# Kernel tuning notes

Measured on AMD Instinct MI355X. Metric: run time of the kernel, lower is better.

## Reference

```python
import jax, jax.numpy as jnp
import numpy as np
from functools import partial

B, C, FD, H, W = 8, 256, 128, 64, 64
POSC = 34  # 32 learned pos channels + 2 raw meshgrid channels


def create_meshgrid(h, w):
    # kornia-style normalized grid in [-1, 1], returned as [1, 2, h, w] (x, y)
    xs = jnp.linspace(-1.0, 1.0, w, dtype=jnp.float32)
    ys = jnp.linspace(-1.0, 1.0, h, dtype=jnp.float32)
    gy, gx = jnp.meshgrid(ys, xs, indexing='ij')
    return jnp.stack([gx, gy], axis=0)[None]  # [1,2,h,w]


def conv1x1(x, w, b):
    return jnp.einsum('bchw,oc->bohw', x, w) + b[None, :, None, None]


def pos_gen(feat, pg_w1, pg_b1, pg_w2, pg_b2):
    # PosGen type=2 with detach: two 1x1 'mul' layers (conv + ReLU, no norm)
    b, c, h, w = feat.shape
    feat = jax.lax.stop_gradient(feat)
    pos = jnp.broadcast_to(create_meshgrid(h, w), (b, 2, h, w))
    inp = jnp.concatenate([pos + 1.0, feat], axis=1)           # [b, feat_dim+2, h, w]
    h1 = jax.nn.relu(conv1x1(inp, pg_w1, pg_b1))               # [b, feat_dim, h, w]
    h2 = jax.nn.relu(conv1x1(h1, pg_w2, pg_b2))                # [b, 32, h, w]
    return jnp.concatenate([h2, pos], axis=1)                  # [b, 34, h, w]


def fuser(x, feat, w1, b1, w2, b2):
    # fuser_1D: concat along channels, 1x1 -> hidden (ReLU) -> 1x1 -> 256
    z = jnp.concatenate([x, feat], axis=1)
    z = jax.nn.relu(conv1x1(z, w1, b1))
    return conv1x1(z, w2, b2)


def conv_y(y, dw_w, dw_b, pw_w, pw_b):
    # BasicDWLayer: depthwise 3x3 + pointwise 1x1, no norm, no activation
    z = jax.lax.conv_general_dilated(
        y, dw_w, window_strides=(1, 1), padding='SAME',
        feature_group_count=y.shape[1],
        dimension_numbers=('NCHW', 'OIHW', 'NCHW')) + dw_b[None, :, None, None]
    return conv1x1(z, pw_w, pw_b)


def matching_forward(x, y, feat1, feat2,
                     pg_w1, pg_b1, pg_w2, pg_b2,
                     fus_w1, fus_b1, fus_w2, fus_b2,
                     dw_w, dw_b, pw_w, pw_b,
                     dustbin_vec, dustbin_pos):
    b, c, hx, wx = x.shape
    hy, wy = y.shape[2], y.shape[3]

    posf = pos_gen(feat2, pg_w1, pg_b1, pg_w2, pg_b2)          # [b, 34, hy, wy]
    c_pose = posf.shape[1]
    pos = posf.reshape(b, 1, c_pose, hy * wy).swapaxes(-1, -2)  # [b,1,Nk,34]

    xf = fuser(x, feat1, fus_w1, fus_b1, fus_w2, fus_b2)
    yf = fuser(y, feat2, fus_w1, fus_b1, fus_w2, fus_b2)
    yf = conv_y(yf, dw_w, dw_b, pw_w, pw_b)
    d = yf.shape[1]

    q = xf.reshape(b, 1, d, hx * wx).swapaxes(-1, -2)           # [b,1,Nq,256]
    k = yf.reshape(b, 1, d, hy * wy).swapaxes(-1, -2)           # [b,1,Nk,256]

    # dustbin token augmentation
    k = jnp.concatenate([k, jnp.broadcast_to(dustbin_vec, (b, 1, 1, d))], axis=-2)
    pos = jnp.concatenate([pos, jnp.broadcast_to(dustbin_pos, (b, 1, 1, c_pose))], axis=-2)

    # single-head cross-attention: values are the positional channels
    scores = jnp.einsum('bhqc,bhkc->bhqk', q, k) / jnp.sqrt(jnp.float32(d))
    attn = jax.nn.softmax(scores, axis=-1)
    out = jnp.einsum('bhqk,bhkd->bhqd', attn, pos)              # [b,1,Nq,34]
    return out.swapaxes(-1, -2).reshape(b, c_pose, hx, wx)


def setup_inputs() -> dict:
    key = jax.random.key(0)
    ks = jax.random.split(key, 20)
    s = 0.05
    return {
        'x': jax.random.normal(ks[0], (B, C, H, W), jnp.float32),
        'y': jax.random.normal(ks[1], (B, C, H, W), jnp.float32),
        'feat1': jax.random.normal(ks[2], (B, FD, H, W), jnp.float32),
        'feat2': jax.random.normal(ks[3], (B, FD, H, W), jnp.float32),
        # PosGen type-2 mapping: (feat_dim+2)->feat_dim, feat_dim->(hidden-2=32)
        'pg_w1': jax.random.normal(ks[4], (FD, FD + 2), jnp.float32) * s,
        'pg_b1': jnp.zeros((FD,), jnp.float32),
        'pg_w2': jax.random.normal(ks[5], (32, FD), jnp.float32) * s,
        'pg_b2': jnp.zeros((32,), jnp.float32),
        # fuser_1D: (256+128)->256 hidden, hidden->256
        'fus_w1': jax.random.normal(ks[6], (256, C + FD), jnp.float32) * s,
        'fus_b1': jnp.zeros((256,), jnp.float32),
        'fus_w2': jax.random.normal(ks[7], (C, 256), jnp.float32) * s,
        'fus_b2': jnp.zeros((C,), jnp.float32),
        # conv_y: depthwise 3x3 + pointwise 1x1
        'dw_w': jax.random.normal(ks[8], (C, 1, 3, 3), jnp.float32) * s,
        'dw_b': jnp.zeros((C,), jnp.float32),
        'pw_w': jax.random.normal(ks[9], (C, C), jnp.float32) * s,
        'pw_b': jnp.zeros((C,), jnp.float32),
        'dustbin_vec': jax.random.uniform(ks[10], (1, 1, 1, C), jnp.float32) / 10.0,
        'dustbin_pos': jnp.zeros((1, 1, 1, POSC), jnp.float32) - 10.0,
    }


def reference(x, y, feat1, feat2,
              pg_w1, pg_b1, pg_w2, pg_b2,
              fus_w1, fus_b1, fus_w2, fus_b2,
              dw_w, dw_b, pw_w, pw_b,
              dustbin_vec, dustbin_pos):
    return matching_forward(x, y, feat1, feat2,
                            pg_w1, pg_b1, pg_w2, pg_b2,
                            fus_w1, fus_b1, fus_w2, fus_b2,
                            dw_w, dw_b, pw_w, pw_b,
                            dustbin_vec, dustbin_pos)
```

## Files before the change

### kernel.cpp

```cpp
#include <hip/hip_runtime.h>
#include <hip/hip_bf16.h>

typedef __hip_bfloat16 bf16;
typedef unsigned short ushort_t;
typedef __bf16 bf16x8 __attribute__((ext_vector_type(8)));
typedef float  f32x4  __attribute__((ext_vector_type(4)));

#define HW    4096
#define NB    8
#define KSTR  4160
#define NTOK  32768
#define PROWS 64
#define QSCALE 0.0901684400557f

__device__ __forceinline__ float lde(const void* p, size_t i, int f32f) {
    return f32f ? ((const float*)p)[i] : (float)((const bf16*)p)[i];
}
__device__ __forceinline__ ushort_t f2bu(float f){ union { __bf16 b; ushort_t u; } cv; cv.b = (__bf16)f; return cv.u; }

__device__ __forceinline__ void async_cp16(const void* g, void* l) {
    __builtin_amdgcn_global_load_lds(
        (const __attribute__((address_space(1))) unsigned int*)g,
        (__attribute__((address_space(3))) unsigned int*)l, 16, 0, 0);
}

__global__ void detect_kernel(const ushort_t* xb, int* flag)
{
    __shared__ int cnt;
    const int t = threadIdx.x;
    if (t == 0) cnt = 0;
    __syncthreads();
    ushort_t h = xb[2*t];
    int e = (h >> 7) & 0xFF;
    if (e >= 133) atomicAdd(&cnt, 1);
    __syncthreads();
    if (t == 0) *flag = (cnt > 8) ? 1 : 0;
}

struct WsPtrs {
    bf16 *fw1t, *fw2t, *pwt, *pgw1t, *pgw2t, *dwt, *pos;
    float *posw, *fb1, *fb2, *pwb, *pgb1, *pgb2, *dwb;
};

__global__ __launch_bounds__(256) void prep_kernel(
    const void* fus_w1, const void* fus_w2, const void* pw_w,
    const void* pg_w1, const void* pg_w2, const void* dw_w,
    const void* fus_b1, const void* fus_b2, const void* pw_b,
    const void* pg_b1, const void* pg_b2, const void* dw_b,
    const void* dpos, WsPtrs W, const int* flag)
{
    const int f = *flag;
    const long n_w1 = 98304, n_w2 = 65536, n_pw = 65536, n_g1 = 16384, n_g2 = 4096;
    const long n_posw = 256, n_dwt = 2304;
    const long n_b = 256, n_gb1 = 128, n_gb2 = 32;
    const long n_mesh = 65536;
    const long n_pad  = 8L*14*KSTR;
    const long n_dust = 272;
    const long n_zt   = 8L*34*63;
    const long total = n_w1+n_w2+n_pw+n_g1+n_g2+n_posw+n_dwt
                     + 3*n_b + n_gb1 + n_gb2 + n_b + n_mesh + n_pad + n_dust + n_zt;

    for (long i = blockIdx.x*256L + threadIdx.x; i < total; i += gridDim.x*256L) {
        long j = i;
        if (j < n_w1) { W.fw1t[j] = __float2bfloat16(lde(fus_w1, j, f)); continue; } j -= n_w1;
        if (j < n_w2) { W.fw2t[j] = __float2bfloat16(lde(fus_w2, j, f)); continue; } j -= n_w2;
        if (j < n_pw) { W.pwt[j]  = __float2bfloat16(lde(pw_w,  j, f)); continue; } j -= n_pw;
        if (j < n_g1) { W.pgw1t[j] = __float2bfloat16(lde(pg_w1, (j>>7)*130 + 2 + (j&127), f)); continue; } j -= n_g1;
        if (j < n_g2) { W.pgw2t[j] = __float2bfloat16(lde(pg_w2, j, f)); continue; } j -= n_g2;
        if (j < n_posw) { W.posw[j] = lde(pg_w1, (j>>1)*130 + (j&1), f); continue; } j -= n_posw;
        if (j < n_dwt) { W.dwt[j] = __float2bfloat16(lde(dw_w, (j&255)*9 + (j>>8), f)); continue; } j -= n_dwt;
        if (j < n_b)   { W.fb1[j] = lde(fus_b1, j, f); continue; } j -= n_b;
        if (j < n_b)   { W.fb2[j] = lde(fus_b2, j, f); continue; } j -= n_b;
        if (j < n_b)   { W.pwb[j] = lde(pw_b, j, f); continue; } j -= n_b;
        if (j < n_gb1) { W.pgb1[j] = lde(pg_b1, j, f); continue; } j -= n_gb1;
        if (j < n_gb2) { W.pgb2[j] = lde(pg_b2, j, f); continue; } j -= n_gb2;
        if (j < n_b)   { W.dwb[j] = lde(dw_b, j, f); continue; } j -= n_b;
        if (j < n_mesh) {
            long b = j >> 13; int rr = (int)((j>>12)&1); int tok = (int)(j & 4095);
            float v = rr ? (-1.f + 2.f*(float)((tok>>6)&63)/63.f)
                         : (-1.f + 2.f*(float)(tok&63)/63.f);
            W.pos[((size_t)b*PROWS + 32 + rr)*KSTR + tok] = __float2bfloat16(v);
            continue;
        } j -= n_mesh;
        if (j < n_pad) {
            long b = j / (14L*KSTR); long rem = j % (14L*KSTR);
            int row = 34 + (int)(rem / KSTR); int tok = (int)(rem % KSTR);
            W.pos[((size_t)b*PROWS + row)*KSTR + tok] = __float2bfloat16(row == 34 ? 1.f : 0.f);
            continue;
        } j -= n_pad;
        if (j < n_dust) {
            long b = j / 34; int ch = (int)(j % 34);
            W.pos[((size_t)b*PROWS + ch)*KSTR + 4096] = __float2bfloat16(lde(dpos, ch, f));
            continue;
        } j -= n_dust;
        { long b = j / (34*63); long rem = j % (34*63);
          int ch = (int)(rem / 63); int cc = (int)(rem % 63);
          W.pos[((size_t)b*PROWS + ch)*KSTR + 4097 + cc] = __float2bfloat16(0.f); }
    }
}

__global__ __launch_bounds__(256) void transpose_kernel(
    const void* main_src, const void* feat_src, bf16* __restrict__ dst, const int* flag)
{
    __shared__ float Tt[64*65];
    const int t = threadIdx.x;
    const int p0 = blockIdx.x * 64;
    const int cht = blockIdx.y;
    const int b = blockIdx.z;
    const int f = *flag;

    const void* src; int ch0, srcC, dc0;
    if (cht < 4) { src = main_src; ch0 = cht*64; srcC = 256; dc0 = ch0; }
    else         { src = feat_src; ch0 = (cht-4)*64; srcC = 128; dc0 = 256 + (cht-4)*64; }

    const int p = t & 63, cq = t >> 6;
    #pragma unroll
    for (int e = 0; e < 16; ++e) {
        int c = e*4 + cq;
        Tt[p*65 + c] = lde(src, ((size_t)b*srcC + ch0 + c)*HW + p0 + p, f);
    }
    __syncthreads();
    const int pr = t >> 2, cs = (t & 3) * 16;
    union { uint4 u4[2]; ushort_t us[16]; } pk;
    #pragma unroll
    for (int u = 0; u < 16; ++u) pk.us[u] = f2bu(Tt[pr*65 + cs + u]);
    ushort_t* op = (ushort_t*)dst + ((size_t)b*HW + p0 + pr)*384 + dc0 + cs;
    *(uint4*)op = pk.u4[0];
    *((uint4*)op + 1) = pk.u4[1];
}

template<int MT, bool RELU, bool POSEPI, int OMODE>
__global__ __launch_bounds__(256) void gemm_mfma(
    const bf16* __restrict__ A, int sa,
    const bf16* __restrict__ Bw, int ldb,
    const float* __restrict__ bias, const float* __restrict__ posw,
    bf16* __restrict__ out, int sm, int K, float oscale)
{
    const int t = threadIdx.x;
    const int w = t >> 6, lane = t & 63;
    const int n = lane & 15, quad = lane >> 4;
    const int p0 = blockIdx.x * 128;
    const int m0 = blockIdx.y * (MT*16);
    const int rowbase = p0 + w*32;

    f32x4 acc[2][MT];
    #pragma unroll
    for (int pt = 0; pt < 2; ++pt)
        #pragma unroll
        for (int mt = 0; mt < MT; ++mt) acc[pt][mt] = (f32x4){0.f,0.f,0.f,0.f};

    for (int k0 = 0; k0 < K; k0 += 32) {
        bf16x8 ap[2];
        #pragma unroll
        for (int pt = 0; pt < 2; ++pt)
            ap[pt] = *(const bf16x8*)&A[(size_t)(rowbase + pt*16 + n)*sa + k0 + quad*8];
        #pragma unroll
        for (int mt = 0; mt < MT; ++mt) {
            bf16x8 bw = *(const bf16x8*)&Bw[(size_t)(m0 + mt*16 + n)*ldb + k0 + quad*8];
            acc[0][mt] = __builtin_amdgcn_mfma_f32_16x16x32_bf16(ap[0], bw, acc[0][mt], 0, 0, 0);
            acc[1][mt] = __builtin_amdgcn_mfma_f32_16x16x32_bf16(ap[1], bw, acc[1][mt], 0, 0, 0);
        }
    }

    #pragma unroll
    for (int mt = 0; mt < MT; ++mt) {
        const int m = m0 + mt*16 + n;
        const float bi = bias[m];
        float w0 = 0.f, w1 = 0.f;
        if (POSEPI) { w0 = posw[m*2]; w1 = posw[m*2 + 1]; }
        #pragma unroll
        for (int pt = 0; pt < 2; ++pt) {
            const int tokb = rowbase + pt*16 + quad*4;
            if (OMODE == 1) {
                union { uint2 u2; ushort_t us[4]; } pk;
                #pragma unroll
                for (int r = 0; r < 4; ++r) {
                    float v = acc[pt][mt][r] + bi;
                    if (RELU) v = fmaxf(v, 0.f);
                    pk.us[r] = f2bu(v * oscale);
                }
                size_t oi = ((size_t)(tokb >> 12)*PROWS + m)*KSTR + (tokb & 4095);
                *(uint2*)((ushort_t*)out + oi) = pk.u2;
            } else {
                #pragma unroll
                for (int r = 0; r < 4; ++r) {
                    int tok = tokb + r;
                    float v = acc[pt][mt][r] + bi;
                    if (POSEPI) {
                        float gx1 = 2.f * (float)(tok & 63) / 63.f;
                        float gy1 = 2.f * (float)((tok >> 6) & 63) / 63.f;
                        v += w0*gx1 + w1*gy1;
                    }
                    if (RELU) v = fmaxf(v, 0.f);
                    v *= oscale;
                    size_t row = (OMODE == 2) ? (size_t)tok + 64*(size_t)(tok >> 12) : (size_t)tok;
                    out[row*sm + m] = __float2bfloat16(v);
                }
            }
        }
    }
}

__global__ __launch_bounds__(256) void dw_kernel(
    const bf16* __restrict__ in, const bf16* __restrict__ dwt,
    const float* __restrict__ dwb, bf16* __restrict__ out)
{
    const int t = threadIdx.x;
    const int tok = blockIdx.x*8 + (t >> 5);
    const int c8 = (t & 31) * 8;
    const int b = tok >> 12, p = tok & 4095;
    const int i = p >> 6, j = p & 63;

    float acc[8];
    #pragma unroll
    for (int u = 0; u < 8; ++u) acc[u] = dwb[c8 + u];

    #pragma unroll
    for (int di = 0; di < 3; ++di) {
        int ii = i + di - 1;
        if (ii < 0 || ii >= 64) continue;
        #pragma unroll
        for (int dj = 0; dj < 3; ++dj) {
            int jj = j + dj - 1;
            if (jj < 0 || jj >= 64) continue;
            int tok2 = (b << 12) + ii*64 + jj;
            bf16x8 xv = *(const bf16x8*)&in[(size_t)tok2*256 + c8];
            bf16x8 wv = *(const bf16x8*)&dwt[(di*3 + dj)*256 + c8];
            #pragma unroll
            for (int u = 0; u < 8; ++u) acc[u] += (float)xv[u] * (float)wv[u];
        }
    }
    union { uint4 u4; ushort_t us[8]; } pk;
    #pragma unroll
    for (int u = 0; u < 8; ++u) pk.us[u] = f2bu(acc[u]);
    *(uint4*)((ushort_t*)out + (size_t)tok*256 + c8) = pk.u4;
}

__global__ __launch_bounds__(256) void fill_late_kernel(
    const void* dvec, bf16* __restrict__ k_t, const int* flag)
{
    const int b = blockIdx.x, t = threadIdx.x;
    k_t[((size_t)b*KSTR + 4096)*256 + t] = __float2bfloat16(lde(dvec, t, *flag));
}

__global__ __launch_bounds__(256, 2) void attn_kernel(
    const bf16* __restrict__ q_t, const bf16* __restrict__ k_t,
    const bf16* __restrict__ pos, void* outv, const int* flag)
{
    __shared__ __align__(16) __bf16 Ks[2048*8];
    __shared__ __align__(16) __bf16 posb[512*8];
    __shared__ __align__(16) __bf16 Pb[64*72];

    const int t = threadIdx.x;
    const int w = t >> 6, lane = t & 63;
    const int n = lane & 15, quad = lane >> 4;
    const int qt = blockIdx.x, b = blockIdx.y;

    bf16x8 aq[8];
    {
        size_t qrow = (size_t)b*HW + qt*64 + w*16 + n;
        #pragma unroll
        for (int c = 0; c < 8; ++c)
            aq[c] = *(const bf16x8*)&q_t[qrow*256 + c*32 + quad*8];
    }

    f32x4 pacc[3];
    #pragma unroll
    for (int ct = 0; ct < 3; ++ct) pacc[ct] = (f32x4){0.f,0.f,0.f,0.f};

    const ushort_t* ksrc0 = (const ushort_t*)k_t + (size_t)b*KSTR*256;
    const ushort_t* psrc0 = (const ushort_t*)pos + (size_t)b*PROWS*KSTR;
    const int xw = n & 7;

    for (int kt = 0; kt < 65; ++kt) {
        const int kbase = kt*64;

        __syncthreads();
        #pragma unroll
        for (int e = 0; e < 8; ++e) {
            int slot = w*512 + e*64 + lane;
            int tok = slot >> 5;
            int ch = ((slot & 31) ^ (tok & 7)) * 8;
            async_cp16(&ksrc0[(size_t)(kbase + tok)*256 + ch], &Ks[(size_t)slot*8]);
        }
        #pragma unroll
        for (int e = 0; e < 2; ++e) {
            int slot = w*128 + e*64 + lane;
            int row = slot >> 3;
            int ch = ((slot & 7) ^ (row & 7)) * 8;
            async_cp16(&psrc0[(size_t)row*KSTR + kbase + ch], &posb[(size_t)slot*8]);
        }
        __syncthreads();

        f32x4 sacc[4];
        #pragma unroll
        for (int nt = 0; nt < 4; ++nt) sacc[nt] = (f32x4){0.f,0.f,0.f,0.f};
        #pragma unroll
        for (int c = 0; c < 8; ++c) {
            #pragma unroll
            for (int nt = 0; nt < 4; ++nt) {
                bf16x8 bk = *(const bf16x8*)&Ks[(size_t)((nt*16 + n)*32 + ((c*4 + quad) ^ xw))*8];
                sacc[nt] = __builtin_amdgcn_mfma_f32_16x16x32_bf16(aq[c], bk, sacc[nt], 0, 0, 0);
            }
        }

        #pragma unroll
        for (int nt = 0; nt < 4; ++nt) {
            const bool ok = (kbase + nt*16 + n) <= 4096;
            #pragma unroll
            for (int r = 0; r < 4; ++r) {
                float pv = ok ? __builtin_amdgcn_exp2f(sacc[nt][r]) : 0.f;
                Pb[(w*16 + quad*4 + r)*72 + nt*16 + n] = (__bf16)pv;
            }
        }

        #pragma unroll
        for (int c = 0; c < 2; ++c) {
            bf16x8 aP = *(const bf16x8*)&Pb[(w*16 + n)*72 + c*32 + quad*8];
            #pragma unroll
            for (int ct = 0; ct < 3; ++ct) {
                bf16x8 bp = *(const bf16x8*)&posb[(size_t)((ct*16 + n)*8 + ((c*4 + quad) ^ xw))*8];
                pacc[ct] = __builtin_amdgcn_mfma_f32_16x16x32_bf16(aP, bp, pacc[ct], 0, 0, 0);
            }
        }
    }

    const int f32o = *flag;
    float linv[4];
    #pragma unroll
    for (int r = 0; r < 4; ++r)
        linv[r] = 1.f / __shfl(pacc[2][r], (lane & 48) | 2, 64);
    #pragma unroll
    for (int ct = 0; ct < 3; ++ct) {
        int ch = ct*16 + n;
        if (ch >= 34) continue;
        #pragma unroll
        for (int r = 0; r < 4; ++r) {
            float v = pacc[ct][r] * linv[r];
            size_t oi = ((size_t)b*34 + ch)*HW + qt*64 + w*16 + quad*4 + r;
            if (f32o) ((float*)outv)[oi] = v;
            else      ((bf16*)outv)[oi]  = __float2bfloat16(v);
        }
    }
}

extern "C" void kernel_launch(void* const* d_in, const int* in_sizes, int n_in,
                              void* d_out, int out_size, void* d_ws, size_t ws_size,
                              hipStream_t stream)
{
    const void* x      = d_in[0];
    const void* y      = d_in[1];
    const void* feat1  = d_in[2];
    const void* feat2  = d_in[3];
    const void* pg_w1  = d_in[4];
    const void* pg_b1  = d_in[5];
    const void* pg_w2  = d_in[6];
    const void* pg_b2  = d_in[7];
    const void* fus_w1 = d_in[8];
    const void* fus_b1 = d_in[9];
    const void* fus_w2 = d_in[10];
    const void* fus_b2 = d_in[11];
    const void* dw_w   = d_in[12];
    const void* dw_b   = d_in[13];
    const void* pw_w   = d_in[14];
    const void* pw_b   = d_in[15];
    const void* dvec   = d_in[16];
    const void* dpos   = d_in[17];

    char* wsb = (char*)d_ws;
    int*  flag = (int*)wsb;
    size_t off = 16;
    bf16* R1   = (bf16*)(wsb + off); off += (size_t)NTOK*384*2;
    bf16* bufH = (bf16*)(wsb + off); off += (size_t)NTOK*256*2;
    bf16* q_t  = (bf16*)(wsb + off); off += (size_t)NTOK*256*2;
    bf16* pos  = (bf16*)(wsb + off); off += (size_t)NB*PROWS*KSTR*2;
    WsPtrs W;
    W.fw1t  = (bf16*)(wsb + off); off += 98304*2;
    W.fw2t  = (bf16*)(wsb + off); off += 65536*2;
    W.pwt   = (bf16*)(wsb + off); off += 65536*2;
    W.pgw1t = (bf16*)(wsb + off); off += 16384*2;
    W.pgw2t = (bf16*)(wsb + off); off += 4096*2;
    W.dwt   = (bf16*)(wsb + off); off += 2304*2;
    W.pos   = pos;
    W.posw  = (float*)(wsb + off); off += 256*4;
    W.fb1   = (float*)(wsb + off); off += 256*4;
    W.fb2   = (float*)(wsb + off); off += 256*4;
    W.pwb   = (float*)(wsb + off); off += 256*4;
    W.pgb1  = (float*)(wsb + off); off += 128*4;
    W.pgb2  = (float*)(wsb + off); off += 32*4;
    W.dwb   = (float*)(wsb + off); off += 256*4;

    bf16* in_xy = R1;
    bf16* yf    = R1;
    bf16* k_t   = R1;

    dim3 b256(256);

    detect_kernel<<<1, 256, 0, stream>>>((const ushort_t*)x, flag);
    prep_kernel<<<1024, b256, 0, stream>>>(fus_w1, fus_w2, pw_w, pg_w1, pg_w2, dw_w,
                                           fus_b1, fus_b2, pw_b, pg_b1, pg_b2, dw_b,
                                           dpos, W, flag);
    transpose_kernel<<<dim3(64,6,NB), b256, 0, stream>>>(x, feat1, in_xy, flag);
    gemm_mfma<8, true, false, 0><<<dim3(256,2), b256, 0, stream>>>(
        in_xy, 384, W.fw1t, 384, W.fb1, nullptr, bufH, 256, 384, 1.f);
    gemm_mfma<8, false, false, 0><<<dim3(256,2), b256, 0, stream>>>(
        bufH, 256, W.fw2t, 256, W.fb2, nullptr, q_t, 256, 256, QSCALE);
    transpose_kernel<<<dim3(64,6,NB), b256, 0, stream>>>(y, feat2, in_xy, flag);
    gemm_mfma<8, true, true, 0><<<dim3(256,1), b256, 0, stream>>>(
        in_xy + 256, 384, W.pgw1t, 128, W.pgb1, W.posw, bufH, 128, 128, 1.f);
    gemm_mfma<2, true, false, 1><<<dim3(256,1), b256, 0, stream>>>(
        bufH, 128, W.pgw2t, 128, W.pgb2, nullptr, pos, 0, 128, 1.f);
    gemm_mfma<8, true, false, 0><<<dim3(256,2), b256, 0, stream>>>(
        in_xy, 384, W.fw1t, 384, W.fb1, nullptr, bufH, 256, 384, 1.f);
    gemm_mfma<8, false, false, 0><<<dim3(256,2), b256, 0, stream>>>(
        bufH, 256, W.fw2t, 256, W.fb2, nullptr, yf, 256, 256, 1.f);
    dw_kernel<<<dim3(4096), b256, 0, stream>>>(yf, W.dwt, W.dwb, bufH);
    fill_late_kernel<<<dim3(NB), b256, 0, stream>>>(dvec, k_t, flag);
    gemm_mfma<8, false, false, 2><<<dim3(256,2), b256, 0, stream>>>(
        bufH, 256, W.pwt, 256, W.pwb, nullptr, k_t, 256, 256, 1.f);
    attn_kernel<<<dim3(64,NB), b256, 0, stream>>>(q_t, k_t, pos, d_out, flag);
}
```

Baseline: 498.4 us.

## Split attention keys across waves with LDS reduction; prefetch GEMM operands

The attention kernel no longer stages K and pos tiles through shared memory with block-wide barriers. Each wave now holds all 64 queries in registers, streams its own slice of keys directly from global memory, and the four waves' partial accumulators are summed through LDS at the end. The pos buffer stride is padded to 4224 so the new 128-key stepping stays in bounds, and the padding is zero-filled. The GEMM kernel gains register double-buffering of its A/B operands and runs with MT=4 on twice as many blocks. Risks: more register pressure and vector loads in attention, K reads that run past each batch's rows (masked by the validity check), and an extra LDS reduction pass.

```diff
diff --git a/kernel.cpp b/kernel.cpp
--- a/kernel.cpp
+++ b/kernel.cpp
@@ -9,20 +9,14 @@
 #define HW    4096
 #define NB    8
 #define KSTR  4160
+#define PSTR  4224
 #define NTOK  32768
-#define PROWS 64
 #define QSCALE 0.0901684400557f
 
 __device__ __forceinline__ float lde(const void* p, size_t i, int f32f) {
     return f32f ? ((const float*)p)[i] : (float)((const bf16*)p)[i];
 }
 __device__ __forceinline__ ushort_t f2bu(float f){ union { __bf16 b; ushort_t u; } cv; cv.b = (__bf16)f; return cv.u; }
-
-__device__ __forceinline__ void async_cp16(const void* g, void* l) {
-    __builtin_amdgcn_global_load_lds(
-        (const __attribute__((address_space(1))) unsigned int*)g,
-        (__attribute__((address_space(3))) unsigned int*)l, 16, 0, 0);
-}
 
 __global__ void detect_kernel(const ushort_t* xb, int* flag)
 {
@@ -54,9 +48,9 @@
     const long n_posw = 256, n_dwt = 2304;
     const long n_b = 256, n_gb1 = 128, n_gb2 = 32;
     const long n_mesh = 65536;
-    const long n_pad  = 8L*14*KSTR;
+    const long n_pad  = 8L*14*PSTR;
     const long n_dust = 272;
-    const long n_zt   = 8L*34*63;
+    const long n_zt   = 8L*34*127;
     const long total = n_w1+n_w2+n_pw+n_g1+n_g2+n_posw+n_dwt
                      + 3*n_b + n_gb1 + n_gb2 + n_b + n_mesh + n_pad + n_dust + n_zt;
 
@@ -79,23 +73,24 @@
             long b = j >> 13; int rr = (int)((j>>12)&1); int tok = (int)(j & 4095);
             float v = rr ? (-1.f + 2.f*(float)((tok>>6)&63)/63.f)
                          : (-1.f + 2.f*(float)(tok&63)/63.f);
-            W.pos[((size_t)b*PROWS + 32 + rr)*KSTR + tok] = __float2bfloat16(v);
+            W.pos[((size_t)b*64 + 32 + rr)*PSTR + tok] = __float2bfloat16(v);
             continue;
         } j -= n_mesh;
         if (j < n_pad) {
-            long b = j / (14L*KSTR); long rem = j % (14L*KSTR);
-            int row = 34 + (int)(rem / KSTR); int tok = (int)(rem % KSTR);
-            W.pos[((size_t)b*PROWS + row)*KSTR + tok] = __float2bfloat16(row == 34 ? 1.f : 0.f);
+            long b = j / (14L*PSTR); long rem = j % (14L*PSTR);
+            int row = 34 + (int)(rem / PSTR); int tok = (int)(rem % PSTR);
+            float v = (row == 34 && tok <= 4096) ? 1.f : 0.f;
+            W.pos[((size_t)b*64 + row)*PSTR + tok] = __float2bfloat16(v);
             continue;
         } j -= n_pad;
         if (j < n_dust) {
             long b = j / 34; int ch = (int)(j % 34);
-            W.pos[((size_t)b*PROWS + ch)*KSTR + 4096] = __float2bfloat16(lde(dpos, ch, f));
+            W.pos[((size_t)b*64 + ch)*PSTR + 4096] = __float2bfloat16(lde(dpos, ch, f));
             continue;
         } j -= n_dust;
-        { long b = j / (34*63); long rem = j % (34*63);
-          int ch = (int)(rem / 63); int cc = (int)(rem % 63);
-          W.pos[((size_t)b*PROWS + ch)*KSTR + 4097 + cc] = __float2bfloat16(0.f); }
+        { long b = j / (34*127); long rem = j % (34*127);
+          int ch = (int)(rem / 127); int cc = (int)(rem % 127);
+          W.pos[((size_t)b*64 + ch)*PSTR + 4097 + cc] = __float2bfloat16(0.f); }
     }
 }
 
@@ -149,17 +144,33 @@
         #pragma unroll
         for (int mt = 0; mt < MT; ++mt) acc[pt][mt] = (f32x4){0.f,0.f,0.f,0.f};
 
+    const bf16* Ar0 = A + (size_t)(rowbase + n)*sa + quad*8;
+    const bf16* Ar1 = A + (size_t)(rowbase + 16 + n)*sa + quad*8;
+
+    bf16x8 a0 = *(const bf16x8*)Ar0;
+    bf16x8 a1 = *(const bf16x8*)Ar1;
+    bf16x8 bw[MT];
+    #pragma unroll
+    for (int mt = 0; mt < MT; ++mt)
+        bw[mt] = *(const bf16x8*)&Bw[(size_t)(m0 + mt*16 + n)*ldb + quad*8];
+
+    const int kmax = K - 32;
     for (int k0 = 0; k0 < K; k0 += 32) {
-        bf16x8 ap[2];
-        #pragma unroll
-        for (int pt = 0; pt < 2; ++pt)
-            ap[pt] = *(const bf16x8*)&A[(size_t)(rowbase + pt*16 + n)*sa + k0 + quad*8];
+        const int kn = (k0 < kmax) ? k0 + 32 : k0;
+        bf16x8 na0 = *(const bf16x8*)(Ar0 + kn);
+        bf16x8 na1 = *(const bf16x8*)(Ar1 + kn);
+        bf16x8 nbw[MT];
+        #pragma unroll
+        for (int mt = 0; mt < MT; ++mt)
+            nbw[mt] = *(const bf16x8*)&Bw[(size_t)(m0 + mt*16 + n)*ldb + kn + quad*8];
         #pragma unroll
         for (int mt = 0; mt < MT; ++mt) {
-            bf16x8 bw = *(const bf16x8*)&Bw[(size_t)(m0 + mt*16 + n)*ldb + k0 + quad*8];
-            acc[0][mt] = __builtin_amdgcn_mfma_f32_16x16x32_bf16(ap[0], bw, acc[0][mt], 0, 0, 0);
-            acc[1][mt] = __builtin_amdgcn_mfma_f32_16x16x32_bf16(ap[1], bw, acc[1][mt], 0, 0, 0);
-        }
+            acc[0][mt] = __builtin_amdgcn_mfma_f32_16x16x32_bf16(a0, bw[mt], acc[0][mt], 0, 0, 0);
+            acc[1][mt] = __builtin_amdgcn_mfma_f32_16x16x32_bf16(a1, bw[mt], acc[1][mt], 0, 0, 0);
+        }
+        a0 = na0; a1 = na1;
+        #pragma unroll
+        for (int mt = 0; mt < MT; ++mt) bw[mt] = nbw[mt];
     }
 
     #pragma unroll
@@ -179,7 +190,7 @@
                     if (RELU) v = fmaxf(v, 0.f);
                     pk.us[r] = f2bu(v * oscale);
                 }
-                size_t oi = ((size_t)(tokb >> 12)*PROWS + m)*KSTR + (tokb & 4095);
+                size_t oi = ((size_t)(tokb >> 12)*64 + m)*PSTR + (tokb & 4095);
                 *(uint2*)((ushort_t*)out + oi) = pk.u2;
             } else {
                 #pragma unroll
@@ -247,96 +258,104 @@
     const bf16* __restrict__ q_t, const bf16* __restrict__ k_t,
     const bf16* __restrict__ pos, void* outv, const int* flag)
 {
-    __shared__ __align__(16) __bf16 Ks[2048*8];
-    __shared__ __align__(16) __bf16 posb[512*8];
-    __shared__ __align__(16) __bf16 Pb[64*72];
+    __shared__ __align__(16) float red[4*12*64*4];
+    __shared__ __align__(16) __bf16 Pb[4*64*40];
 
     const int t = threadIdx.x;
     const int w = t >> 6, lane = t & 63;
     const int n = lane & 15, quad = lane >> 4;
     const int qt = blockIdx.x, b = blockIdx.y;
 
-    bf16x8 aq[8];
-    {
-        size_t qrow = (size_t)b*HW + qt*64 + w*16 + n;
+    bf16x8 aq[4][8];
+    #pragma unroll
+    for (int q2 = 0; q2 < 4; ++q2) {
+        size_t qrow = (size_t)b*HW + qt*64 + q2*16 + n;
         #pragma unroll
         for (int c = 0; c < 8; ++c)
-            aq[c] = *(const bf16x8*)&q_t[qrow*256 + c*32 + quad*8];
-    }
-
-    f32x4 pacc[3];
-    #pragma unroll
-    for (int ct = 0; ct < 3; ++ct) pacc[ct] = (f32x4){0.f,0.f,0.f,0.f};
-
-    const ushort_t* ksrc0 = (const ushort_t*)k_t + (size_t)b*KSTR*256;
-    const ushort_t* psrc0 = (const ushort_t*)pos + (size_t)b*PROWS*KSTR;
-    const int xw = n & 7;
-
-    for (int kt = 0; kt < 65; ++kt) {
-        const int kbase = kt*64;
-
-        __syncthreads();
-        #pragma unroll
-        for (int e = 0; e < 8; ++e) {
-            int slot = w*512 + e*64 + lane;
-            int tok = slot >> 5;
-            int ch = ((slot & 31) ^ (tok & 7)) * 8;
-            async_cp16(&ksrc0[(size_t)(kbase + tok)*256 + ch], &Ks[(size_t)slot*8]);
-        }
-        #pragma unroll
-        for (int e = 0; e < 2; ++e) {
-            int slot = w*128 + e*64 + lane;
-            int row = slot >> 3;
-            int ch = ((slot & 7) ^ (row & 7)) * 8;
-            async_cp16(&psrc0[(size_t)row*KSTR + kbase + ch], &posb[(size_t)slot*8]);
-        }
-        __syncthreads();
-
-        f32x4 sacc[4];
-        #pragma unroll
-        for (int nt = 0; nt < 4; ++nt) sacc[nt] = (f32x4){0.f,0.f,0.f,0.f};
-        #pragma unroll
-        for (int c = 0; c < 8; ++c) {
-            #pragma unroll
-            for (int nt = 0; nt < 4; ++nt) {
-                bf16x8 bk = *(const bf16x8*)&Ks[(size_t)((nt*16 + n)*32 + ((c*4 + quad) ^ xw))*8];
-                sacc[nt] = __builtin_amdgcn_mfma_f32_16x16x32_bf16(aq[c], bk, sacc[nt], 0, 0, 0);
-            }
-        }
-
-        #pragma unroll
-        for (int nt = 0; nt < 4; ++nt) {
-            const bool ok = (kbase + nt*16 + n) <= 4096;
-            #pragma unroll
-            for (int r = 0; r < 4; ++r) {
-                float pv = ok ? __builtin_amdgcn_exp2f(sacc[nt][r]) : 0.f;
-                Pb[(w*16 + quad*4 + r)*72 + nt*16 + n] = (__bf16)pv;
-            }
-        }
-
-        #pragma unroll
-        for (int c = 0; c < 2; ++c) {
-            bf16x8 aP = *(const bf16x8*)&Pb[(w*16 + n)*72 + c*32 + quad*8];
-            #pragma unroll
-            for (int ct = 0; ct < 3; ++ct) {
-                bf16x8 bp = *(const bf16x8*)&posb[(size_t)((ct*16 + n)*8 + ((c*4 + quad) ^ xw))*8];
-                pacc[ct] = __builtin_amdgcn_mfma_f32_16x16x32_bf16(aP, bp, pacc[ct], 0, 0, 0);
-            }
-        }
-    }
-
+            aq[q2][c] = *(const bf16x8*)&q_t[qrow*256 + c*32 + quad*8];
+    }
+
+    f32x4 pacc[4][3];
+    #pragma unroll
+    for (int q2 = 0; q2 < 4; ++q2)
+        #pragma unroll
+        for (int ct = 0; ct < 3; ++ct) pacc[q2][ct] = (f32x4){0.f,0.f,0.f,0.f};
+
+    const bf16* kb0 = k_t + (size_t)b*KSTR*256;
+    const bf16* pb0 = pos + (size_t)b*64*PSTR;
+    __bf16* Pw = Pb + w*64*40;
+
+    for (int i = 0; i < 33; ++i) {
+        const int base = i*128 + w*32;
+
+        #pragma unroll
+        for (int nt2 = 0; nt2 < 2; ++nt2) {
+            const int kb = base + nt2*16;
+            bf16x8 bk[8];
+            #pragma unroll
+            for (int c = 0; c < 8; ++c)
+                bk[c] = *(const bf16x8*)&kb0[(size_t)(kb + n)*256 + c*32 + quad*8];
+            f32x4 sacc[4];
+            #pragma unroll
+            for (int q2 = 0; q2 < 4; ++q2) sacc[q2] = (f32x4){0.f,0.f,0.f,0.f};
+            #pragma unroll
+            for (int c = 0; c < 8; ++c)
+                #pragma unroll
+                for (int q2 = 0; q2 < 4; ++q2)
+                    sacc[q2] = __builtin_amdgcn_mfma_f32_16x16x32_bf16(aq[q2][c], bk[c], sacc[q2], 0, 0, 0);
+            const bool ok = (kb + n) <= 4096;
+            #pragma unroll
+            for (int q2 = 0; q2 < 4; ++q2)
+                #pragma unroll
+                for (int r = 0; r < 4; ++r) {
+                    float pv = ok ? __builtin_amdgcn_exp2f(sacc[q2][r]) : 0.f;
+                    Pw[(q2*16 + quad*4 + r)*40 + nt2*16 + n] = (__bf16)pv;
+                }
+        }
+
+        bf16x8 bp[3];
+        #pragma unroll
+        for (int ct = 0; ct < 3; ++ct)
+            bp[ct] = *(const bf16x8*)&pb0[(size_t)(ct*16 + n)*PSTR + base + quad*8];
+
+        #pragma unroll
+        for (int q2 = 0; q2 < 4; ++q2) {
+            bf16x8 aP = *(const bf16x8*)&Pw[(q2*16 + n)*40 + quad*8];
+            #pragma unroll
+            for (int ct = 0; ct < 3; ++ct)
+                pacc[q2][ct] = __builtin_amdgcn_mfma_f32_16x16x32_bf16(aP, bp[ct], pacc[q2][ct], 0, 0, 0);
+        }
+    }
+
+    #pragma unroll
+    for (int q2 = 0; q2 < 4; ++q2)
+        #pragma unroll
+        for (int ct = 0; ct < 3; ++ct)
+            *(f32x4*)&red[(((w*12) + q2*3 + ct)*64 + lane)*4] = pacc[q2][ct];
+    __syncthreads();
+
+    f32x4 sum[3];
+    #pragma unroll
+    for (int ct = 0; ct < 3; ++ct) {
+        sum[ct] = (f32x4){0.f,0.f,0.f,0.f};
+        #pragma unroll
+        for (int w2 = 0; w2 < 4; ++w2) {
+            f32x4 v = *(const f32x4*)&red[(((w2*12) + w*3 + ct)*64 + lane)*4];
+            sum[ct] += v;
+        }
+    }
     const int f32o = *flag;
     float linv[4];
     #pragma unroll
     for (int r = 0; r < 4; ++r)
-        linv[r] = 1.f / __shfl(pacc[2][r], (lane & 48) | 2, 64);
+        linv[r] = 1.f / __shfl(sum[2][r], (lane & 48) | 2, 64);
     #pragma unroll
     for (int ct = 0; ct < 3; ++ct) {
         int ch = ct*16 + n;
         if (ch >= 34) continue;
         #pragma unroll
         for (int r = 0; r < 4; ++r) {
-            float v = pacc[ct][r] * linv[r];
+            float v = sum[ct][r] * linv[r];
             size_t oi = ((size_t)b*34 + ch)*HW + qt*64 + w*16 + quad*4 + r;
             if (f32o) ((float*)outv)[oi] = v;
             else      ((bf16*)outv)[oi]  = __float2bfloat16(v);
@@ -373,7 +392,7 @@
     bf16* R1   = (bf16*)(wsb + off); off += (size_t)NTOK*384*2;
     bf16* bufH = (bf16*)(wsb + off); off += (size_t)NTOK*256*2;
     bf16* q_t  = (bf16*)(wsb + off); off += (size_t)NTOK*256*2;
-    bf16* pos  = (bf16*)(wsb + off); off += (size_t)NB*PROWS*KSTR*2;
+    bf16* pos  = (bf16*)(wsb + off); off += (size_t)NB*64*PSTR*2;
     WsPtrs W;
     W.fw1t  = (bf16*)(wsb + off); off += 98304*2;
     W.fw2t  = (bf16*)(wsb + off); off += 65536*2;
@@ -401,22 +420,22 @@
                                            fus_b1, fus_b2, pw_b, pg_b1, pg_b2, dw_b,
                                            dpos, W, flag);
     transpose_kernel<<<dim3(64,6,NB), b256, 0, stream>>>(x, feat1, in_xy, flag);
-    gemm_mfma<8, true, false, 0><<<dim3(256,2), b256, 0, stream>>>(
+    gemm_mfma<4, true, false, 0><<<dim3(256,4), b256, 0, stream>>>(
         in_xy, 384, W.fw1t, 384, W.fb1, nullptr, bufH, 256, 384, 1.f);
-    gemm_mfma<8, false, false, 0><<<dim3(256,2), b256, 0, stream>>>(
+    gemm_mfma<4, false, false, 0><<<dim3(256,4), b256, 0, stream>>>(
         bufH, 256, W.fw2t, 256, W.fb2, nullptr, q_t, 256, 256, QSCALE);
     transpose_kernel<<<dim3(64,6,NB), b256, 0, stream>>>(y, feat2, in_xy, flag);
-    gemm_mfma<8, true, true, 0><<<dim3(256,1), b256, 0, stream>>>(
+    gemm_mfma<4, true, true, 0><<<dim3(256,2), b256, 0, stream>>>(
         in_xy + 256, 384, W.pgw1t, 128, W.pgb1, W.posw, bufH, 128, 128, 1.f);
     gemm_mfma<2, true, false, 1><<<dim3(256,1), b256, 0, stream>>>(
         bufH, 128, W.pgw2t, 128, W.pgb2, nullptr, pos, 0, 128, 1.f);
-    gemm_mfma<8, true, false, 0><<<dim3(256,2), b256, 0, stream>>>(
+    gemm_mfma<4, true, false, 0><<<dim3(256,4), b256, 0, stream>>>(
         in_xy, 384, W.fw1t, 384, W.fb1, nullptr, bufH, 256, 384, 1.f);
-    gemm_mfma<8, false, false, 0><<<dim3(256,2), b256, 0, stream>>>(
+    gemm_mfma<4, false, false, 0><<<dim3(256,4), b256, 0, stream>>>(
         bufH, 256, W.fw2t, 256, W.fb2, nullptr, yf, 256, 256, 1.f);
     dw_kernel<<<dim3(4096), b256, 0, stream>>>(yf, W.dwt, W.dwb, bufH);
     fill_late_kernel<<<dim3(NB), b256, 0, stream>>>(dvec, k_t, flag);
-    gemm_mfma<8, false, false, 2><<<dim3(256,2), b256, 0, stream>>>(
+    gemm_mfma<4, false, false, 2><<<dim3(256,4), b256, 0, stream>>>(
         bufH, 256, W.pwt, 256, W.pwb, nullptr, k_t, 256, 256, 1.f);
     attn_kernel<<<dim3(64,NB), b256, 0, stream>>>(q_t, k_t, pos, d_out, flag);
 }
```

Result: slower. 545.1 us (+9.4%).
